# Performance work log

Measured on AMD Instinct MI355X. Metric: run time of the kernel, lower is better.

The kernel has to match this reference:

```python
import jax, jax.numpy as jnp
import numpy as np

N = 8192
IN_CH = 128
OUT_CH = 64
HEADS = 2
NEG_SLOPE = 0.2


def setup_inputs() -> dict:
    key = jax.random.key(0)
    k1, k2, k3, k4, k5 = jax.random.split(key, 5)
    A = jax.random.uniform(k1, (N, N), dtype=jnp.float32)  # dense weighted adjacency
    X = jax.random.normal(k2, (N, IN_CH), dtype=jnp.float32)
    # Parameters match torch init: rand(...) / 10
    W = jax.random.uniform(k3, (IN_CH, OUT_CH, HEADS), dtype=jnp.float32) / 10.0
    attn = jax.random.uniform(k4, (2 * OUT_CH, HEADS), dtype=jnp.float32) / 10.0
    b = jax.random.uniform(k5, (HEADS, OUT_CH), dtype=jnp.float32) / 10.0
    return {"A": A, "X": X, "W": W, "attn": attn, "b": b}


def reference(A, X, W, attn, b):
    # Project: [N, in] x [in, out, H] -> [N, out, H]
    Xp = jnp.einsum('ik,kjl->ijl', X, W)
    # Per-node attention halves: [N, H]
    X0 = jnp.einsum('ijk,jk->ik', Xp, attn[:OUT_CH, :])
    X1 = jnp.einsum('ijk,jk->ik', Xp, attn[OUT_CH:, :])
    # Pairwise scores [N, N, H]: dst i (X0) + src j (X1)
    S = X0[:, None, :] + X1[None, :, :]
    E = jnp.exp(jax.nn.leaky_relu(S, negative_slope=NEG_SLOPE))
    # Mask by adjacency: [N, N, H]
    Aw = A[:, :, None] * E
    # Row-normalize over neighbor axis (dim 1) with epsilon 0.001
    d = 1.0 / (jnp.sum(Aw, axis=1) + 0.001)  # [N, H]
    Aw = d[:, None, :] * Aw
    # Aggregate: [N,N,H] x [N,out,H] -> [N, H, out], add bias [H, out]
    out = jnp.einsum('ikl,kjl->ilj', Aw, Xp) + b
    return out
```

## Files before the change

kernel.cpp:

```cpp
#include <hip/hip_runtime.h>
#include <hip/hip_bf16.h>

typedef unsigned short ushort_t;
typedef unsigned int uint_t;
using f32x4  = __attribute__((ext_vector_type(4))) float;
using short8 = __attribute__((ext_vector_type(8))) short;

#define NN 8192

__device__ __forceinline__ ushort_t f2bf(float f) {
  uint_t u = __builtin_bit_cast(uint_t, f);
  u += 0x7FFFu + ((u >> 16) & 1u);
  return (ushort_t)(u >> 16);
}

__device__ __forceinline__ void gload16(const void* g, void* l) {
  __builtin_amdgcn_global_load_lds(
      (const __attribute__((address_space(1))) void*)g,
      (__attribute__((address_space(3))) void*)l, 16, 0, 0);
}

__global__ __launch_bounds__(256, 2) void k1_project(
    const float* __restrict__ X, const float* __restrict__ W,
    const float* __restrict__ attn,
    ushort_t* __restrict__ XpT, float* __restrict__ x0g, float* __restrict__ x1g)
{
  __shared__ float    Xl[32][128];
  __shared__ ushort_t XpL[128][56];
  __shared__ float    P0[128][33];
  __shared__ float    P1[128][33];
  const int t  = threadIdx.x;
  const int nb = blockIdx.x * 32;

  #pragma unroll
  for (int r = 0; r < 4; ++r) {
    int chunk = r * 256 + t;
    ((float4*)(&Xl[0][0]))[chunk] = ((const float4*)(X + (size_t)nb * 128))[chunk];
  }
  __syncthreads();

  const int p = t & 127;
  const int g = t >> 7;
  const int h = p & 1, c = p >> 1;

  float acc[16];
  #pragma unroll
  for (int n = 0; n < 16; ++n) acc[n] = 0.f;

  for (int jc = 0; jc < 4; ++jc) {
    float wreg[32];
    #pragma unroll
    for (int jj = 0; jj < 32; ++jj) wreg[jj] = W[(jc * 32 + jj) * 128 + p];
    #pragma unroll
    for (int n = 0; n < 16; ++n) {
      const float4* xr = (const float4*)(&Xl[g * 16 + n][jc * 32]);
      float s = acc[n];
      #pragma unroll
      for (int q = 0; q < 8; ++q) {
        float4 xv = xr[q];
        s += xv.x * wreg[q*4+0] + xv.y * wreg[q*4+1] + xv.z * wreg[q*4+2] + xv.w * wreg[q*4+3];
      }
      acc[n] = s;
    }
  }

  const float a0 = attn[p];
  const float a1 = attn[128 + p];
  const int   row = h * 64 + c;
  #pragma unroll
  for (int n = 0; n < 16; ++n) {
    P0[p][g * 16 + n]  = acc[n] * a0;
    P1[p][g * 16 + n]  = acc[n] * a1;
    XpL[row][g * 16 + n] = f2bf(acc[n]);
  }
  __syncthreads();

  if (t < 128) {
    ushort_t* dst = XpT + (size_t)t * NN + nb;
    const uint4* src = (const uint4*)(&XpL[t][0]);
    ((uint4*)dst)[0] = src[0];
    ((uint4*)dst)[1] = src[1];
    ((uint4*)dst)[2] = src[2];
    ((uint4*)dst)[3] = src[3];
  }
  if (t < 64) {
    int node = t >> 1, hh = t & 1;
    float s0 = 0.f, s1 = 0.f;
    #pragma unroll
    for (int cc = 0; cc < 64; ++cc) {
      s0 += P0[cc * 2 + hh][node];
      s1 += P1[cc * 2 + hh][node];
    }
    x0g[(nb + node) * 2 + hh] = s0;
    x1g[hh * NN + nb + node]  = s1;
  }
}

__global__ __launch_bounds__(256, 4) void k2_main(
    const float* __restrict__ A, const ushort_t* __restrict__ XpT,
    const float* __restrict__ x0g, const float* __restrict__ x1g,
    float* __restrict__ part, float* __restrict__ denp,
    const int S, const int KS)
{
  __shared__ __align__(16) ushort_t Pl[64 * 64];
  __shared__ __align__(16) ushort_t Bl[2 * 128 * 64];
  const int t  = threadIdx.x;
  const int b  = blockIdx.x;
  const int rb = b / S, sp = b % S;
  const int ib = rb * 32;
  const int k0 = sp * KS;
  const int lane = t & 63, w = t >> 6;
  const int hw = w & 1, iw = (w >> 1) * 16;
  const int pr = t >> 4;
  const int pk = (t & 15) * 4;

  float x0a[2][2];
  #pragma unroll
  for (int ps = 0; ps < 2; ++ps) {
    float2 v = *(const float2*)(x0g + (ib + ps * 16 + pr) * 2);
    x0a[ps][0] = v.x; x0a[ps][1] = v.y;
  }

  int srcOff[4], ldsOff[4];
  #pragma unroll
  for (int q = 0; q < 4; ++q) {
    int c = q * 256 + t;
    int cr = c >> 3, j = c & 7;
    srcOff[q] = cr * NN + ((j ^ (cr & 7)) << 3);
    ldsOff[q] = (q * 256 + w * 64) << 3;
  }

  int plw[2][2];
  #pragma unroll
  for (int ps = 0; ps < 2; ++ps)
    #pragma unroll
    for (int hh = 0; hh < 2; ++hh) {
      int row = hh * 32 + ps * 16 + pr;
      plw[ps][hh] = (row * 128 + pk * 2) ^ ((pr & 7) << 4);
    }

  int aoff[2], boff[2][4];
  const int arow = hw * 32 + iw + (lane & 15);
  #pragma unroll
  for (int ks = 0; ks < 2; ++ks) {
    aoff[ks] = (arow * 128 + ks * 64 + (lane >> 4) * 16) ^ ((arow & 7) << 4);
    #pragma unroll
    for (int cb = 0; cb < 4; ++cb) {
      int brow = hw * 64 + cb * 16 + (lane & 15);
      boff[ks][cb] = (brow * 128 + ks * 64 + (lane >> 4) * 16) ^ ((brow & 7) << 4);
    }
  }

  f32x4 acc[4] = {};
  float den[2][2] = {};

  const float* Ap0 = A + (size_t)(ib + pr) * NN + k0 + pk;
  const float* Ap1 = A + (size_t)(ib + 16 + pr) * NN + k0 + pk;
  const float* Xq0 = x1g + k0 + pk;
  const float* Xq1 = x1g + NN + k0 + pk;
  const int nt = KS >> 6;
  const int lastT = nt - 1;

  float4 Ua0 = *(const float4*)(Ap0);
  float4 Ua1 = *(const float4*)(Ap1);
  float4 Ux0 = *(const float4*)(Xq0);
  float4 Ux1 = *(const float4*)(Xq1);
  float4 Va0 = *(const float4*)(Ap0 + 64);
  float4 Va1 = *(const float4*)(Ap1 + 64);
  float4 Vx0 = *(const float4*)(Xq0 + 64);
  float4 Vx1 = *(const float4*)(Xq1 + 64);
  {
    const ushort_t* s = XpT + k0;
    #pragma unroll
    for (int q = 0; q < 4; ++q) gload16(s + srcOff[q], Bl + ldsOff[q]);
  }

#define KBODY(a0v, a1v, x0v, x1v, TT, PAR)                                   \
  {                                                                          \
    const int  t_  = (TT);                                                   \
    const bool pf_ = (t_ + 1 < nt);                                          \
                           \
    float aarr[2][4] = {{a0v.x, a0v.y, a0v.z, a0v.w},                        \
                        {a1v.x, a1v.y, a1v.z, a1v.w}};                       \
    float xarr[2][4] = {{x0v.x, x0v.y, x0v.z, x0v.w},                        \
                        {x1v.x, x1v.y, x1v.z, x1v.w}};                       \
    uint_t pp[2][2][2];                                                      \
    _Pragma("unroll")                                                        \
    for (int ps = 0; ps < 2; ++ps) {                                         \
      _Pragma("unroll")                                                      \
      for (int hh = 0; hh < 2; ++hh) {                                       \
        ushort_t bfv[4];                                                     \
        _Pragma("unroll")                                                    \
        for (int j = 0; j < 4; ++j) {                                        \
          float s   = x0a[ps][hh] + xarr[hh][j];                             \
          float lrl = fmaxf(s, 0.2f * s);                                    \
          float e   = __expf(lrl);                                           \
          float pv  = aarr[ps][j] * e;                                       \
          den[ps][hh] += pv;                                                 \
          bfv[j] = f2bf(pv);                                                 \
        }                                                                    \
        pp[ps][hh][0] = (uint_t)bfv[0] | ((uint_t)bfv[1] << 16);             \
        pp[ps][hh][1] = (uint_t)bfv[2] | ((uint_t)bfv[3] << 16);             \
      }                                                                      \
    }                                                                        \
       \
    asm volatile("s_waitcnt lgkmcnt(0)" ::: "memory");                       \
    __builtin_amdgcn_s_barrier();                                            \
    asm volatile("" ::: "memory");                                           \
                     \
    if (pf_) {                                                               \
      const ushort_t* s_ = XpT + k0 + ((t_ + 1) << 6);                       \
      ushort_t* d_ = Bl + ((PAR) ^ 1) * 8192;                                \
      _Pragma("unroll")                                                      \
      for (int q = 0; q < 4; ++q) gload16(s_ + srcOff[q], d_ + ldsOff[q]);   \
    }                                                                        \
       \
    {                                                                        \
      const int rt_ = (t_ + 2 < nt) ? (t_ + 2) : lastT;                      \
      const int rk_ = rt_ << 6;                                              \
      a0v = *(const float4*)(Ap0 + rk_);                                     \
      a1v = *(const float4*)(Ap1 + rk_);                                     \
      x0v = *(const float4*)(Xq0 + rk_);                                     \
      x1v = *(const float4*)(Xq1 + rk_);                                     \
    }                                                                        \
                                                            \
    _Pragma("unroll")                                                        \
    for (int ps = 0; ps < 2; ++ps) {                                         \
      _Pragma("unroll")                                                      \
      for (int hh = 0; hh < 2; ++hh) {                                       \
        uint2 v_; v_.x = pp[ps][hh][0]; v_.y = pp[ps][hh][1];                \
        *(uint2*)((char*)Pl + plw[ps][hh]) = v_;                             \
      }                                                                      \
    }                                                                        \
        \
    if (pf_) asm volatile("s_waitcnt vmcnt(8) lgkmcnt(0)" ::: "memory");     \
    else     asm volatile("s_waitcnt vmcnt(0) lgkmcnt(0)" ::: "memory");     \
    __builtin_amdgcn_s_barrier();                                            \
    asm volatile("" ::: "memory");                                           \
                                               \
    const char* BlC_ = (const char*)(Bl + (PAR) * 8192);                     \
    _Pragma("unroll")                                                        \
    for (int ks = 0; ks < 2; ++ks) {                                         \
      short8 af = *(const short8*)((const char*)Pl + aoff[ks]);              \
      _Pragma("unroll")                                                      \
      for (int cb = 0; cb < 4; ++cb) {                                       \
        short8 bv = *(const short8*)(BlC_ + boff[ks][cb]);                   \
        acc[cb] = __builtin_amdgcn_mfma_f32_16x16x32_bf16(af, bv, acc[cb], 0, 0, 0); \
      }                                                                      \
    }                                                                        \
  }

  for (int tt = 0; tt < nt; tt += 2) {
    KBODY(Ua0, Ua1, Ux0, Ux1, tt,     0)
    KBODY(Va0, Va1, Vx0, Vx1, tt + 1, 1)
  }
#undef KBODY

  #pragma unroll
  for (int ps = 0; ps < 2; ++ps) {
    #pragma unroll
    for (int hh = 0; hh < 2; ++hh) {
      float d = den[ps][hh];
      d += __shfl_xor(d, 1, 16);
      d += __shfl_xor(d, 2, 16);
      d += __shfl_xor(d, 4, 16);
      d += __shfl_xor(d, 8, 16);
      if ((t & 15) == 0)
        denp[((size_t)sp * NN + ib + ps * 16 + (t >> 4)) * 2 + hh] = d;
    }
  }

  float* pbase = part + ((size_t)sp * NN + ib) * 128;
  #pragma unroll
  for (int cb = 0; cb < 4; ++cb) {
    #pragma unroll
    for (int r = 0; r < 4; ++r) {
      int lr  = iw + (lane >> 4) * 4 + r;
      int col = cb * 16 + (lane & 15);
      pbase[lr * 128 + hw * 64 + col] = acc[cb][r];
    }
  }
}

__global__ __launch_bounds__(256) void k3_finish(
    const float* __restrict__ part, const float* __restrict__ denp,
    const float* __restrict__ bias, float* __restrict__ out, const int S)
{
  const int idx = blockIdx.x * 256 + threadIdx.x;
  const int i  = idx >> 5;
  const int hc = (idx & 31) * 4;
  const int h  = hc >> 6;
  float4 s; s.x = s.y = s.z = s.w = 0.f;
  float d = 0.f;
  for (int sp = 0; sp < S; ++sp) {
    float4 v = *(const float4*)(part + ((size_t)sp * NN + i) * 128 + hc);
    s.x += v.x; s.y += v.y; s.z += v.z; s.w += v.w;
    d += denp[((size_t)sp * NN + i) * 2 + h];
  }
  const float sc = 1.f / (d + 0.001f);
  float4 bv = *(const float4*)(bias + hc);
  float4 o;
  o.x = s.x * sc + bv.x;
  o.y = s.y * sc + bv.y;
  o.z = s.z * sc + bv.z;
  o.w = s.w * sc + bv.w;
  *(float4*)(out + (size_t)i * 128 + hc) = o;
}

extern "C" void kernel_launch(void* const* d_in, const int* in_sizes, int n_in,
                              void* d_out, int out_size, void* d_ws, size_t ws_size,
                              hipStream_t stream) {
  const float* A    = (const float*)d_in[0];
  const float* X    = (const float*)d_in[1];
  const float* W    = (const float*)d_in[2];
  const float* attn = (const float*)d_in[3];
  const float* bias = (const float*)d_in[4];
  float* out = (float*)d_out;

  char* ws = (char*)d_ws;
  size_t off = 0;
  ushort_t* XpT = (ushort_t*)(ws + off); off += (size_t)128 * NN * sizeof(ushort_t);
  float* x0g = (float*)(ws + off); off += (size_t)NN * 2 * sizeof(float);
  float* x1g = (float*)(ws + off); off += (size_t)2 * NN * sizeof(float);

  int S = 4;
  while (S > 1) {
    size_t need = off + (size_t)S * NN * 2 * 4 + (size_t)S * NN * 128 * 4;
    if (need <= ws_size) break;
    S >>= 1;
  }
  float* denp = (float*)(ws + off); off += (size_t)S * NN * 2 * sizeof(float);
  float* part = (float*)(ws + off);
  const int KS = NN / S;

  k1_project<<<256, 256, 0, stream>>>(X, W, attn, XpT, x0g, x1g);
  k2_main<<<256 * S, 256, 0, stream>>>(A, XpT, x0g, x1g, part, denp, S, KS);
  k3_finish<<<1024, 256, 0, stream>>>(part, denp, bias, out, S);
}
```

Measured before the change: 119.7 us.

## Load XpT MFMA operands directly to registers and double-buffer P tile

The main kernel no longer stages the bf16 XpT tile through LDS with global_load_lds. Each wave now loads its B fragments straight into registers, prefetched two tiles ahead, and the wave-to-output mapping changes so each wave covers 2x2 blocks instead of 1x4. The P tile in LDS is double-buffered, which cuts the per-tile barriers from two to one. The exponential becomes a raw v_exp_f32 with log2(e) folded into the attention weights in the projection kernel, and bf16 packing uses v_cvt_pk_bf16_f32. The cost is more VGPR pressure and more redundant global reads of XpT, since waves no longer share it through LDS.

```diff
diff --git a/kernel.cpp b/kernel.cpp
--- a/kernel.cpp
+++ b/kernel.cpp
@@ -7,6 +7,7 @@
 using short8 = __attribute__((ext_vector_type(8))) short;
 
 #define NN 8192
+#define INVLN2 1.4426950408889634f
 
 __device__ __forceinline__ ushort_t f2bf(float f) {
   uint_t u = __builtin_bit_cast(uint_t, f);
@@ -14,10 +15,8 @@
   return (ushort_t)(u >> 16);
 }
 
-__device__ __forceinline__ void gload16(const void* g, void* l) {
-  __builtin_amdgcn_global_load_lds(
-      (const __attribute__((address_space(1))) void*)g,
-      (__attribute__((address_space(3))) void*)l, 16, 0, 0);
+__device__ __forceinline__ float fexp2(float x) {
+  float r; asm("v_exp_f32 %0, %1" : "=v"(r) : "v"(x)); return r;
 }
 
 __global__ __launch_bounds__(256, 2) void k1_project(
@@ -64,8 +63,8 @@
     }
   }
 
-  const float a0 = attn[p];
-  const float a1 = attn[128 + p];
+  const float a0 = attn[p] * INVLN2;
+  const float a1 = attn[128 + p] * INVLN2;
   const int   row = h * 64 + c;
   #pragma unroll
   for (int n = 0; n < 16; ++n) {
@@ -102,32 +101,23 @@
     float* __restrict__ part, float* __restrict__ denp,
     const int S, const int KS)
 {
-  __shared__ __align__(16) ushort_t Pl[64 * 64];
-  __shared__ __align__(16) ushort_t Bl[2 * 128 * 64];
+  __shared__ __align__(16) ushort_t Pl[2 * 64 * 64];
   const int t  = threadIdx.x;
   const int b  = blockIdx.x;
   const int rb = b / S, sp = b % S;
   const int ib = rb * 32;
   const int k0 = sp * KS;
   const int lane = t & 63, w = t >> 6;
-  const int hw = w & 1, iw = (w >> 1) * 16;
-  const int pr = t >> 4;
-  const int pk = (t & 15) * 4;
+  const int hw  = w & 1;
+  const int cbh = w >> 1;
+  const int pr  = t >> 4;
+  const int pk  = (t & 15) * 4;
 
   float x0a[2][2];
   #pragma unroll
   for (int ps = 0; ps < 2; ++ps) {
     float2 v = *(const float2*)(x0g + (ib + ps * 16 + pr) * 2);
     x0a[ps][0] = v.x; x0a[ps][1] = v.y;
-  }
-
-  int srcOff[4], ldsOff[4];
-  #pragma unroll
-  for (int q = 0; q < 4; ++q) {
-    int c = q * 256 + t;
-    int cr = c >> 3, j = c & 7;
-    srcOff[q] = cr * NN + ((j ^ (cr & 7)) << 3);
-    ldsOff[q] = (q * 256 + w * 64) << 3;
   }
 
   int plw[2][2];
@@ -139,19 +129,21 @@
       plw[ps][hh] = (row * 128 + pk * 2) ^ ((pr & 7) << 4);
     }
 
-  int aoff[2], boff[2][4];
-  const int arow = hw * 32 + iw + (lane & 15);
-  #pragma unroll
-  for (int ks = 0; ks < 2; ++ks) {
-    aoff[ks] = (arow * 128 + ks * 64 + (lane >> 4) * 16) ^ ((arow & 7) << 4);
-    #pragma unroll
-    for (int cb = 0; cb < 4; ++cb) {
-      int brow = hw * 64 + cb * 16 + (lane & 15);
-      boff[ks][cb] = (brow * 128 + ks * 64 + (lane >> 4) * 16) ^ ((brow & 7) << 4);
-    }
-  }
-
-  f32x4 acc[4] = {};
+  int aoff[2][2];
+  #pragma unroll
+  for (int iwi = 0; iwi < 2; ++iwi) {
+    int arow = hw * 32 + iwi * 16 + (lane & 15);
+    #pragma unroll
+    for (int ks = 0; ks < 2; ++ks)
+      aoff[iwi][ks] = (arow * 128 + ks * 64 + (lane >> 4) * 16) ^ ((arow & 7) << 4);
+  }
+
+  const ushort_t* Bp00 = XpT + (size_t)(hw * 64 + (cbh * 2 + 0) * 16 + (lane & 15)) * NN + k0 +  0 + (lane >> 4) * 8;
+  const ushort_t* Bp01 = XpT + (size_t)(hw * 64 + (cbh * 2 + 1) * 16 + (lane & 15)) * NN + k0 +  0 + (lane >> 4) * 8;
+  const ushort_t* Bp10 = Bp00 + 32;
+  const ushort_t* Bp11 = Bp01 + 32;
+
+  f32x4 acc[2][2] = {};
   float den[2][2] = {};
 
   const float* Ap0 = A + (size_t)(ib + pr) * NN + k0 + pk;
@@ -161,100 +153,80 @@
   const int nt = KS >> 6;
   const int lastT = nt - 1;
 
-  float4 Ua0 = *(const float4*)(Ap0);
-  float4 Ua1 = *(const float4*)(Ap1);
-  float4 Ux0 = *(const float4*)(Xq0);
-  float4 Ux1 = *(const float4*)(Xq1);
-  float4 Va0 = *(const float4*)(Ap0 + 64);
-  float4 Va1 = *(const float4*)(Ap1 + 64);
-  float4 Vx0 = *(const float4*)(Xq0 + 64);
-  float4 Vx1 = *(const float4*)(Xq1 + 64);
-  {
-    const ushort_t* s = XpT + k0;
-    #pragma unroll
-    for (int q = 0; q < 4; ++q) gload16(s + srcOff[q], Bl + ldsOff[q]);
-  }
-
-#define KBODY(a0v, a1v, x0v, x1v, TT, PAR)                                   \
+  float4 Ua0, Ua1, Va0, Va1;
+  short8 Ub00, Ub01, Ub10, Ub11, Vb00, Vb01, Vb10, Vb11;
+
+#define LDA(a0v, a1v, TILE) { const int kk_ = (TILE) << 6;                   \
+    a0v = *(const float4*)(Ap0 + kk_); a1v = *(const float4*)(Ap1 + kk_); }
+#define LDB(q00, q01, q10, q11, TILE) { const int kk_ = (TILE) << 6;         \
+    q00 = *(const short8*)(Bp00 + kk_); q01 = *(const short8*)(Bp01 + kk_);  \
+    q10 = *(const short8*)(Bp10 + kk_); q11 = *(const short8*)(Bp11 + kk_); }
+
+  LDA(Ua0, Ua1, 0) LDB(Ub00, Ub01, Ub10, Ub11, 0)
+  LDA(Va0, Va1, 1) LDB(Vb00, Vb01, Vb10, Vb11, 1)
+
+#define KBODY(a0v, a1v, q00, q01, q10, q11, TT)                              \
   {                                                                          \
-    const int  t_  = (TT);                                                   \
-    const bool pf_ = (t_ + 1 < nt);                                          \
-                           \
+    const int t_  = (TT);                                                    \
+    const int rt_ = (t_ + 2 < nt) ? (t_ + 2) : lastT;                        \
+    char* plb = (char*)Pl + (t_ & 1) * 8192;                                 \
+                                   \
+    float4 xv0 = *(const float4*)(Xq0 + (t_ << 6));                          \
+    float4 xv1 = *(const float4*)(Xq1 + (t_ << 6));                          \
     float aarr[2][4] = {{a0v.x, a0v.y, a0v.z, a0v.w},                        \
                         {a1v.x, a1v.y, a1v.z, a1v.w}};                       \
-    float xarr[2][4] = {{x0v.x, x0v.y, x0v.z, x0v.w},                        \
-                        {x1v.x, x1v.y, x1v.z, x1v.w}};                       \
-    uint_t pp[2][2][2];                                                      \
+    float xarr[2][4] = {{xv0.x, xv0.y, xv0.z, xv0.w},                        \
+                        {xv1.x, xv1.y, xv1.z, xv1.w}};                       \
     _Pragma("unroll")                                                        \
     for (int ps = 0; ps < 2; ++ps) {                                         \
       _Pragma("unroll")                                                      \
       for (int hh = 0; hh < 2; ++hh) {                                       \
-        ushort_t bfv[4];                                                     \
+        float pv[4];                                                         \
         _Pragma("unroll")                                                    \
         for (int j = 0; j < 4; ++j) {                                        \
-          float s   = x0a[ps][hh] + xarr[hh][j];                             \
-          float lrl = fmaxf(s, 0.2f * s);                                    \
-          float e   = __expf(lrl);                                           \
-          float pv  = aarr[ps][j] * e;                                       \
-          den[ps][hh] += pv;                                                 \
-          bfv[j] = f2bf(pv);                                                 \
+          float s = x0a[ps][hh] + xarr[hh][j];                               \
+          float e = fexp2(fmaxf(s, 0.2f * s));                               \
+          pv[j] = aarr[ps][j] * e;                                           \
+          den[ps][hh] += pv[j];                                              \
         }                                                                    \
-        pp[ps][hh][0] = (uint_t)bfv[0] | ((uint_t)bfv[1] << 16);             \
-        pp[ps][hh][1] = (uint_t)bfv[2] | ((uint_t)bfv[3] << 16);             \
+        uint_t u0_, u1_;                                                     \
+        asm("v_cvt_pk_bf16_f32 %0, %1, %2" : "=v"(u0_) : "v"(pv[0]), "v"(pv[1])); \
+        asm("v_cvt_pk_bf16_f32 %0, %1, %2" : "=v"(u1_) : "v"(pv[2]), "v"(pv[3])); \
+        uint2 vv_; vv_.x = u0_; vv_.y = u1_;                                 \
+        *(uint2*)(plb + plw[ps][hh]) = vv_;                                  \
       }                                                                      \
     }                                                                        \
-       \
+                 \
+    LDA(a0v, a1v, rt_)                                                       \
     asm volatile("s_waitcnt lgkmcnt(0)" ::: "memory");                       \
     __builtin_amdgcn_s_barrier();                                            \
     asm volatile("" ::: "memory");                                           \
-                     \
-    if (pf_) {                                                               \
-      const ushort_t* s_ = XpT + k0 + ((t_ + 1) << 6);                       \
-      ushort_t* d_ = Bl + ((PAR) ^ 1) * 8192;                                \
-      _Pragma("unroll")                                                      \
-      for (int q = 0; q < 4; ++q) gload16(s_ + srcOff[q], d_ + ldsOff[q]);   \
+                           \
+    {                                                                        \
+      short8 af00 = *(const short8*)(plb + aoff[0][0]);                      \
+      short8 af10 = *(const short8*)(plb + aoff[1][0]);                      \
+      acc[0][0] = __builtin_amdgcn_mfma_f32_16x16x32_bf16(af00, q00, acc[0][0], 0, 0, 0); \
+      acc[0][1] = __builtin_amdgcn_mfma_f32_16x16x32_bf16(af00, q01, acc[0][1], 0, 0, 0); \
+      acc[1][0] = __builtin_amdgcn_mfma_f32_16x16x32_bf16(af10, q00, acc[1][0], 0, 0, 0); \
+      acc[1][1] = __builtin_amdgcn_mfma_f32_16x16x32_bf16(af10, q01, acc[1][1], 0, 0, 0); \
+      short8 af01 = *(const short8*)(plb + aoff[0][1]);                      \
+      short8 af11 = *(const short8*)(plb + aoff[1][1]);                      \
+      acc[0][0] = __builtin_amdgcn_mfma_f32_16x16x32_bf16(af01, q10, acc[0][0], 0, 0, 0); \
+      acc[0][1] = __builtin_amdgcn_mfma_f32_16x16x32_bf16(af01, q11, acc[0][1], 0, 0, 0); \
+      acc[1][0] = __builtin_amdgcn_mfma_f32_16x16x32_bf16(af11, q10, acc[1][0], 0, 0, 0); \
+      acc[1][1] = __builtin_amdgcn_mfma_f32_16x16x32_bf16(af11, q11, acc[1][1], 0, 0, 0); \
     }                                                                        \
-       \
-    {                                                                        \
-      const int rt_ = (t_ + 2 < nt) ? (t_ + 2) : lastT;                      \
-      const int rk_ = rt_ << 6;                                              \
-      a0v = *(const float4*)(Ap0 + rk_);                                     \
-      a1v = *(const float4*)(Ap1 + rk_);                                     \
-      x0v = *(const float4*)(Xq0 + rk_);                                     \
-      x1v = *(const float4*)(Xq1 + rk_);                                     \
-    }                                                                        \
-                                                            \
-    _Pragma("unroll")                                                        \
-    for (int ps = 0; ps < 2; ++ps) {                                         \
-      _Pragma("unroll")                                                      \
-      for (int hh = 0; hh < 2; ++hh) {                                       \
-        uint2 v_; v_.x = pp[ps][hh][0]; v_.y = pp[ps][hh][1];                \
-        *(uint2*)((char*)Pl + plw[ps][hh]) = v_;                             \
-      }                                                                      \
-    }                                                                        \
-        \
-    if (pf_) asm volatile("s_waitcnt vmcnt(8) lgkmcnt(0)" ::: "memory");     \
-    else     asm volatile("s_waitcnt vmcnt(0) lgkmcnt(0)" ::: "memory");     \
-    __builtin_amdgcn_s_barrier();                                            \
-    asm volatile("" ::: "memory");                                           \
-                                               \
-    const char* BlC_ = (const char*)(Bl + (PAR) * 8192);                     \
-    _Pragma("unroll")                                                        \
-    for (int ks = 0; ks < 2; ++ks) {                                         \
-      short8 af = *(const short8*)((const char*)Pl + aoff[ks]);              \
-      _Pragma("unroll")                                                      \
-      for (int cb = 0; cb < 4; ++cb) {                                       \
-        short8 bv = *(const short8*)(BlC_ + boff[ks][cb]);                   \
-        acc[cb] = __builtin_amdgcn_mfma_f32_16x16x32_bf16(af, bv, acc[cb], 0, 0, 0); \
-      }                                                                      \
-    }                                                                        \
+                                      \
+    LDB(q00, q01, q10, q11, rt_)                                             \
   }
 
   for (int tt = 0; tt < nt; tt += 2) {
-    KBODY(Ua0, Ua1, Ux0, Ux1, tt,     0)
-    KBODY(Va0, Va1, Vx0, Vx1, tt + 1, 1)
+    KBODY(Ua0, Ua1, Ub00, Ub01, Ub10, Ub11, tt)
+    KBODY(Va0, Va1, Vb00, Vb01, Vb10, Vb11, tt + 1)
   }
 #undef KBODY
+#undef LDB
+#undef LDA
 
   #pragma unroll
   for (int ps = 0; ps < 2; ++ps) {
@@ -272,14 +244,15 @@
 
   float* pbase = part + ((size_t)sp * NN + ib) * 128;
   #pragma unroll
-  for (int cb = 0; cb < 4; ++cb) {
-    #pragma unroll
-    for (int r = 0; r < 4; ++r) {
-      int lr  = iw + (lane >> 4) * 4 + r;
-      int col = cb * 16 + (lane & 15);
-      pbase[lr * 128 + hw * 64 + col] = acc[cb][r];
-    }
-  }
+  for (int iwi = 0; iwi < 2; ++iwi)
+    #pragma unroll
+    for (int c = 0; c < 2; ++c)
+      #pragma unroll
+      for (int r = 0; r < 4; ++r) {
+        int lr  = iwi * 16 + (lane >> 4) * 4 + r;
+        int col = (cbh * 2 + c) * 16 + (lane & 15);
+        pbase[lr * 128 + hw * 64 + col] = acc[iwi][c][r];
+      }
 }
 
 __global__ __launch_bounds__(256) void k3_finish(
```

Result: slower. 123.3 us (+3.0%).
